# Kernel tuning notes

Measured on AMD Instinct MI355X. Metric: run time of the kernel, lower is better.

The kernel has to match this reference:

```python
import jax, jax.numpy as jnp
import numpy as np


def setup_inputs() -> dict:
    key = jax.random.key(0)
    ks = jax.random.split(key, 12)
    B, Nv, C, H, W = 4, 4096, 64, 376, 1240
    inp = {
        "voxel_features": jax.random.normal(ks[0], (B, Nv, C), jnp.float32),
        "voxels_3d": jax.random.normal(ks[1], (B, Nv, 3), jnp.float32),
        "img_feats": jax.random.normal(ks[2], (B, C, H, W), jnp.float32),
        "vox_x": jax.random.randint(ks[3], (B, Nv), 0, 1400, jnp.int32),
        "vox_y": jax.random.randint(ks[4], (B, Nv), 0, 430, jnp.int32),
        "q_w": jax.random.normal(ks[5], (C, C), jnp.float32) / np.sqrt(C),
        "q_b": jnp.zeros((C,), jnp.float32),
        "k_w": jax.random.normal(ks[6], (C, 3), jnp.float32) / np.sqrt(3.0),
        "k_b": jnp.zeros((C,), jnp.float32),
        "v_w": jax.random.normal(ks[7], (C, C), jnp.float32) / np.sqrt(C),
        "v_b": jnp.zeros((C,), jnp.float32),
        "o_w": jax.random.normal(ks[8], (C, C), jnp.float32) / np.sqrt(C),
        "o_b": jnp.zeros((C,), jnp.float32),
        "fc_w": jax.random.normal(ks[9], (C, C), jnp.float32) / np.sqrt(C),
    }
    return inp


def reference(voxel_features, voxels_3d, img_feats, vox_x, vox_y,
              q_w, q_b, k_w, k_b, v_w, v_b, o_w, o_b, fc_w):
    # voxel_features: [B, Nv, C] lidar voxel features (value)
    # voxels_3d:      [B, Nv, 3] voxel 3D coords (key)
    # img_feats:      [B, C, H, W] image feature map
    B, C, H, W = img_feats.shape
    Nv = voxel_features.shape[1]

    # --- gather image features at projected voxel pixel coords, zero if OOB ---
    valid = (vox_x >= 0) & (vox_x < W) & (vox_y >= 0) & (vox_y < H)  # [B, Nv]
    xc = jnp.clip(vox_x, 0, W - 1)
    yc = jnp.clip(vox_y, 0, H - 1)
    b_idx = jnp.arange(B)[:, None]
    camera = img_feats[b_idx, :, yc, xc]            # [B, Nv, C]
    camera = jnp.where(valid[..., None], camera, 0.0)

    # --- single-head cross-modal attention (q=camera, k=coords, v=lidar) ---
    scale = 1.0 / jnp.sqrt(jnp.asarray(C, camera.dtype))
    q = (camera @ q_w.T + q_b) * scale              # [B, Nv, C]
    k = voxels_3d @ k_w.T + k_b                     # [B, Nv, C]
    v = voxel_features @ v_w.T + v_b                # [B, Nv, C]
    scores = jnp.einsum('bqc,bkc->bqk', q, k)       # [B, Nv, Nv]
    attn = jax.nn.softmax(scores, axis=-1)
    ctx = jnp.einsum('bqk,bkc->bqc', attn, v)
    ctx = ctx @ o_w.T + o_b                         # out_proj

    fused = jax.nn.relu(ctx @ fc_w.T)               # [B, Nv, C]
    return jnp.concatenate([voxel_features, fused], axis=-1)  # [B, Nv, 2C]
```

## Files before the change

### kernel.cpp

```cpp
#include <hip/hip_runtime.h>

#define BB 4
#define NV 4096
#define BN (BB * NV)
#define CC 64
#define HH 376
#define WW 1240
#define HW (HH * WW)
#define LDT 72
#define LDK 36
#define NSPLIT 4
#define TILES 16
#define QSCALE 0.1803368801111244f

typedef __bf16 bf16x8 __attribute__((ext_vector_type(8)));
typedef __bf16 bf16x4 __attribute__((ext_vector_type(4)));
typedef float  f32x4  __attribute__((ext_vector_type(4)));

__global__ __launch_bounds__(256) void kw2(const float* __restrict__ qw,
                                           const float* __restrict__ qb,
                                           const float* __restrict__ kw,
                                           const float* __restrict__ ow,
                                           const float* __restrict__ ob,
                                           const float* __restrict__ fc,
                                           unsigned short* __restrict__ W2b,
                                           float* __restrict__ b2,
                                           float* __restrict__ Wqk3,
                                           float* __restrict__ bqk3) {
  int idx = blockIdx.x * blockDim.x + threadIdx.x;
  if (idx >= CC * CC) return;
  int i = idx >> 6, j = idx & 63;
  float acc = 0.f;
  for (int k = 0; k < CC; ++k) acc += fc[i * CC + k] * ow[k * CC + j];
  ((__bf16*)W2b)[idx] = (__bf16)acc;
  if (idx < CC) {
    float a = 0.f;
    for (int k = 0; k < CC; ++k) a += fc[idx * CC + k] * ob[k];
    b2[idx] = a;
  }
  if (idx < CC * 3) {
    int jj = idx / 3, d = idx - jj * 3;
    float a = 0.f;
    for (int k = 0; k < CC; ++k) a += qw[k * CC + jj] * kw[k * 3 + d];
    Wqk3[idx] = a;
  }
  if (idx < 3) {
    float a = 0.f;
    for (int k = 0; k < CC; ++k) a += qb[k] * kw[k * 3 + idx];
    bqk3[idx] = a;
  }
}

__global__ __launch_bounds__(256) void kprep(
    const float* __restrict__ vfeat, const float* __restrict__ v3d,
    const float* __restrict__ img, const int* __restrict__ vx,
    const int* __restrict__ vy, const float* __restrict__ Wqk3,
    const float* __restrict__ bqk3, const float* __restrict__ vw,
    const float* __restrict__ vb, float* __restrict__ out,
    unsigned short* __restrict__ Qp, unsigned short* __restrict__ K32,
    unsigned short* __restrict__ VTb) {
  __shared__ float VfS[32][68];
  __shared__ float CamS[32][68];
  const int tid = threadIdx.x;
  const int vl = tid >> 3;
  const int p = tid & 7;
  const int gv = blockIdx.x * 32 + vl;
  const int b = gv >> 12, n = gv & (NV - 1);
  const size_t row = (size_t)b * NV + n;

  {
    const float4* vf4 = (const float4*)(vfeat + row * CC) + p * 2;
    float4* o4 = (float4*)(out + row * 128) + p * 2;
    float4* s4 = (float4*)&VfS[vl][p * 8];
#pragma unroll
    for (int i = 0; i < 2; ++i) { float4 t = vf4[i]; o4[i] = t; s4[i] = t; }
  }

  {
    int x = vx[row], y = vy[row];
    bool valid = (x >= 0) & (x < WW) & (y >= 0) & (y < HH);
    int xs = valid ? x : 0, ys = valid ? y : 0;
    const float* ib = img + ((size_t)b * CC + p * 8) * (size_t)HW + (size_t)ys * WW + xs;
#pragma unroll
    for (int i = 0; i < 8; ++i) {
      float cv = ib[(size_t)i * HW];
      CamS[vl][p * 8 + i] = valid ? cv : 0.f;
    }
  }

  if (p == 0) {
    float c0 = v3d[row * 3 + 0], c1 = v3d[row * 3 + 1], c2 = v3d[row * 3 + 2];
    bf16x8 kp = {(__bf16)c0, (__bf16)c1, (__bf16)c2,
                 (__bf16)0.f, (__bf16)0.f, (__bf16)0.f, (__bf16)0.f, (__bf16)0.f};
    *(bf16x8*)(K32 + row * 32) = kp;
  } else if (p < 4) {
    bf16x8 z = {(__bf16)0.f, (__bf16)0.f, (__bf16)0.f, (__bf16)0.f,
                (__bf16)0.f, (__bf16)0.f, (__bf16)0.f, (__bf16)0.f};
    *(bf16x8*)(K32 + row * 32 + p * 8) = z;
  }
  __syncthreads();

  {
    f32x4 vr[16];
#pragma unroll
    for (int i = 0; i < 16; ++i) vr[i] = *(const f32x4*)&VfS[vl][i * 4];
#pragma unroll
    for (int cc = 0; cc < 8; ++cc) {
      int c = p * 8 + cc;
      const float4* w4 = (const float4*)(vw + c * CC);
      float acc = vb[c];
#pragma unroll
      for (int j = 0; j < 16; ++j) {
        float4 w = w4[j];
        acc = fmaf(vr[j][0], w.x, fmaf(vr[j][1], w.y, fmaf(vr[j][2], w.z, fmaf(vr[j][3], w.w, acc))));
      }
      ((__bf16*)VTb)[((size_t)b * CC + c) * NV + n] = (__bf16)acc;
    }
  }

  if (p == 0) {
    float q0 = bqk3[0], q1 = bqk3[1], q2 = bqk3[2];
#pragma unroll 8
    for (int j = 0; j < CC; ++j) {
      float c = CamS[vl][j];
      q0 = fmaf(c, Wqk3[j * 3 + 0], q0);
      q1 = fmaf(c, Wqk3[j * 3 + 1], q1);
      q2 = fmaf(c, Wqk3[j * 3 + 2], q2);
    }
    bf16x8 qp = {(__bf16)(q0 * QSCALE), (__bf16)(q1 * QSCALE), (__bf16)(q2 * QSCALE),
                 (__bf16)0.f, (__bf16)0.f, (__bf16)0.f, (__bf16)0.f, (__bf16)0.f};
    *(bf16x8*)(Qp + row * 32) = qp;
  } else if (p < 4) {
    bf16x8 z = {(__bf16)0.f, (__bf16)0.f, (__bf16)0.f, (__bf16)0.f,
                (__bf16)0.f, (__bf16)0.f, (__bf16)0.f, (__bf16)0.f};
    *(bf16x8*)(Qp + row * 32 + p * 8) = z;
  }
}

__global__ __launch_bounds__(256, 4) void kattn(const unsigned short* __restrict__ Qp,
                                                const unsigned short* __restrict__ K32,
                                                const unsigned short* __restrict__ VTb,
                                                unsigned short* __restrict__ Opb,
                                                float* __restrict__ ml) {
  __shared__ unsigned short Ks[2][64 * LDK];
  __shared__ unsigned short Vs[2][64 * LDT];
  __shared__ unsigned short Ps[4][16 * LDT];

  const int bid = blockIdx.x;
  const int xcd = bid & 7;
  const int idx = bid >> 3;
  const int combo = xcd * 2 + (idx >> 6);
  const int qc = idx & 63;
  const int b = combo >> 2;
  const int sp = combo & 3;
  const int q0 = qc * 64;
  const int key0 = sp * (TILES * 64);

  const int tid = threadIdx.x;
  const int wid = tid >> 6;
  const int lane = tid & 63;
  const int lq = lane & 15;
  const int lg = lane >> 4;

  const int srow = tid >> 2;
  const int scol = (tid & 3) * 16;
  const int kcol = (tid & 3) * 8;

  bf16x8 qf = *(const bf16x8*)(Qp + ((size_t)b * NV + q0 + wid * 16 + lq) * 32 + lg * 8);

  const f32x4 vzero = {0.f, 0.f, 0.f, 0.f};
  float m_run = -1e30f, l_run = 0.f;
  f32x4 oacc[4];
#pragma unroll
  for (int t = 0; t < 4; ++t) oacc[t] = vzero;

  const unsigned short* kgb = K32 + ((size_t)b * NV) * 32;
  const unsigned short* vgb = VTb + (size_t)b * CC * NV;

  uint4 kq, vr0, vr1;
  {
    kq = *(const uint4*)(kgb + (size_t)(key0 + srow) * 32 + kcol);
    const uint4* vsrc = (const uint4*)(vgb + (size_t)srow * NV + key0 + scol);
    vr0 = vsrc[0]; vr1 = vsrc[1];
    *(uint4*)&Ks[0][srow * LDK + kcol] = kq;
    uint4* vdst = (uint4*)&Vs[0][srow * LDT + scol];
    vdst[0] = vr0; vdst[1] = vr1;
  }
  __syncthreads();

  int cur = 0;
  for (int tt = 0; tt < TILES; ++tt) {
    if (tt + 1 < TILES) {
      int k0 = key0 + (tt + 1) * 64;
      kq = *(const uint4*)(kgb + (size_t)(k0 + srow) * 32 + kcol);
      const uint4* vsrc = (const uint4*)(vgb + (size_t)srow * NV + k0 + scol);
      vr0 = vsrc[0]; vr1 = vsrc[1];
    }

    f32x4 s[4];
#pragma unroll
    for (int t = 0; t < 4; ++t) {
      bf16x8 ka = *(const bf16x8*)&Ks[cur][(t * 16 + lq) * LDK + lg * 8];
      s[t] = __builtin_amdgcn_mfma_f32_16x16x32_bf16(ka, qf, vzero, 0, 0, 0);
    }

    float t0m = fmaxf(fmaxf(s[0][0], s[0][1]), fmaxf(s[0][2], s[0][3]));
    float t1m = fmaxf(fmaxf(s[1][0], s[1][1]), fmaxf(s[1][2], s[1][3]));
    float t2m = fmaxf(fmaxf(s[2][0], s[2][1]), fmaxf(s[2][2], s[2][3]));
    float t3m = fmaxf(fmaxf(s[3][0], s[3][1]), fmaxf(s[3][2], s[3][3]));
    float tmax = fmaxf(fmaxf(t0m, t1m), fmaxf(t2m, t3m));
    tmax = fmaxf(tmax, __shfl_xor(tmax, 16));
    tmax = fmaxf(tmax, __shfl_xor(tmax, 32));

    if (!__all(tmax <= m_run + 8.f)) {
      float m_new = fmaxf(m_run, tmax);
      float sc = __builtin_amdgcn_exp2f(m_run - m_new);
      l_run *= sc;
      m_run = m_new;
#pragma unroll
      for (int r = 0; r < 4; ++r) {
        float scr = __shfl(sc, lg * 4 + r);
#pragma unroll
        for (int t = 0; t < 4; ++t) oacc[t][r] *= scr;
      }
    }

    float psum = 0.f;
#pragma unroll
    for (int t = 0; t < 4; ++t) {
      float p0 = __builtin_amdgcn_exp2f(s[t][0] - m_run);
      float p1 = __builtin_amdgcn_exp2f(s[t][1] - m_run);
      float p2 = __builtin_amdgcn_exp2f(s[t][2] - m_run);
      float p3 = __builtin_amdgcn_exp2f(s[t][3] - m_run);
      psum += (p0 + p1) + (p2 + p3);
      bf16x4 pk;
      pk[0] = (__bf16)p0; pk[1] = (__bf16)p1; pk[2] = (__bf16)p2; pk[3] = (__bf16)p3;
      *(bf16x4*)&Ps[wid][lq * LDT + t * 16 + lg * 4] = pk;
    }
    psum += __shfl_xor(psum, 16);
    psum += __shfl_xor(psum, 32);
    l_run += psum;

#pragma unroll
    for (int ks = 0; ks < 2; ++ks) {
      bf16x8 pa = *(const bf16x8*)&Ps[wid][lq * LDT + ks * 32 + lg * 8];
#pragma unroll
      for (int t = 0; t < 4; ++t) {
        bf16x8 vbf = *(const bf16x8*)&Vs[cur][(t * 16 + lq) * LDT + ks * 32 + lg * 8];
        oacc[t] = __builtin_amdgcn_mfma_f32_16x16x32_bf16(pa, vbf, oacc[t], 0, 0, 0);
      }
    }

    if (tt + 1 < TILES) {
      *(uint4*)&Ks[cur ^ 1][srow * LDK + kcol] = kq;
      uint4* vdst = (uint4*)&Vs[cur ^ 1][srow * LDT + scol];
      vdst[0] = vr0; vdst[1] = vr1;
    }
    __syncthreads();
    cur ^= 1;
  }

  const size_t obase = (size_t)sp * BN + (size_t)b * NV + q0 + wid * 16;
#pragma unroll
  for (int r = 0; r < 4; ++r) {
    __bf16* op = (__bf16*)Opb + (obase + lg * 4 + r) * CC + lq;
#pragma unroll
    for (int t = 0; t < 4; ++t) op[t * 16] = (__bf16)oacc[t][r];
  }
  if (lg == 0) {
    float2 t2; t2.x = m_run; t2.y = l_run;
    ((float2*)ml)[obase + lq] = t2;
  }
}

__global__ __launch_bounds__(256) void kmerge(const unsigned short* __restrict__ Opb,
                                              const float* __restrict__ ml,
                                              const unsigned short* __restrict__ W2b,
                                              const float* __restrict__ b2f,
                                              float* __restrict__ out) {
  __shared__ unsigned short W2s[64 * LDT];
  __shared__ float b2s[64];
  const int tid = threadIdx.x;
  const int wid = tid >> 6;
  const int lane = tid & 63;
  const int lq = lane & 15;
  const int lg = lane >> 4;
  const int srow = tid >> 2;
  const int scol = (tid & 3) * 16;

  {
    const uint4* ws = (const uint4*)(W2b + srow * CC + scol);
    uint4* wd = (uint4*)&W2s[srow * LDT + scol];
    wd[0] = ws[0]; wd[1] = ws[1];
    if (tid < 64) b2s[tid] = b2f[tid];
  }
  __syncthreads();

  const int row = blockIdx.x * 64 + wid * 16 + lq;

  float mv[NSPLIT], lv[NSPLIT], w[NSPLIT];
#pragma unroll
  for (int s = 0; s < NSPLIT; ++s) {
    float2 t = ((const float2*)ml)[(size_t)s * BN + row];
    mv[s] = t.x; lv[s] = t.y;
  }
  float mstar = fmaxf(fmaxf(mv[0], mv[1]), fmaxf(mv[2], mv[3]));
  float lstar = 0.f;
#pragma unroll
  for (int s = 0; s < NSPLIT; ++s) {
    w[s] = __builtin_amdgcn_exp2f(mv[s] - mstar);
    lstar = fmaf(w[s], lv[s], lstar);
  }

  float ctx[16];
#pragma unroll
  for (int j = 0; j < 16; ++j) ctx[j] = 0.f;
#pragma unroll
  for (int s = 0; s < NSPLIT; ++s) {
    const __bf16* oprow = (const __bf16*)Opb + ((size_t)s * BN + row) * CC;
    bf16x8 a0 = *(const bf16x8*)(oprow + lg * 8);
    bf16x8 a1 = *(const bf16x8*)(oprow + 32 + lg * 8);
    float ws_ = w[s];
#pragma unroll
    for (int j = 0; j < 8; ++j) {
      ctx[j] = fmaf(ws_, (float)a0[j], ctx[j]);
      ctx[8 + j] = fmaf(ws_, (float)a1[j], ctx[8 + j]);
    }
  }
  float inv = 1.f / lstar;
  bf16x8 cb0, cb1;
#pragma unroll
  for (int j = 0; j < 8; ++j) {
    cb0[j] = (__bf16)(ctx[j] * inv);
    cb1[j] = (__bf16)(ctx[8 + j] * inv);
  }

  const f32x4 vzero = {0.f, 0.f, 0.f, 0.f};
  float* orow = out + (size_t)row * 128 + 64;
#pragma unroll
  for (int t2 = 0; t2 < 4; ++t2) {
    bf16x8 wa0 = *(const bf16x8*)&W2s[(t2 * 16 + lq) * LDT + lg * 8];
    bf16x8 wa1 = *(const bf16x8*)&W2s[(t2 * 16 + lq) * LDT + 32 + lg * 8];
    f32x4 r2 = vzero;
    r2 = __builtin_amdgcn_mfma_f32_16x16x32_bf16(wa0, cb0, r2, 0, 0, 0);
    r2 = __builtin_amdgcn_mfma_f32_16x16x32_bf16(wa1, cb1, r2, 0, 0, 0);
    float4 o;
    o.x = fmaxf(r2[0] + b2s[t2 * 16 + lg * 4 + 0], 0.f);
    o.y = fmaxf(r2[1] + b2s[t2 * 16 + lg * 4 + 1], 0.f);
    o.z = fmaxf(r2[2] + b2s[t2 * 16 + lg * 4 + 2], 0.f);
    o.w = fmaxf(r2[3] + b2s[t2 * 16 + lg * 4 + 3], 0.f);
    *(float4*)(orow + t2 * 16 + lg * 4) = o;
  }
}

extern "C" void kernel_launch(void* const* d_in, const int* in_sizes, int n_in,
                              void* d_out, int out_size, void* d_ws, size_t ws_size,
                              hipStream_t stream) {
  const float* vfeat = (const float*)d_in[0];
  const float* v3d = (const float*)d_in[1];
  const float* img = (const float*)d_in[2];
  const int* vx = (const int*)d_in[3];
  const int* vy = (const int*)d_in[4];
  const float* qw = (const float*)d_in[5];
  const float* qb = (const float*)d_in[6];
  const float* kw = (const float*)d_in[7];
  const float* kb = (const float*)d_in[8];
  const float* vw = (const float*)d_in[9];
  const float* vb = (const float*)d_in[10];
  const float* ow = (const float*)d_in[11];
  const float* ob = (const float*)d_in[12];
  const float* fc = (const float*)d_in[13];
  float* out = (float*)d_out;
  (void)kb;

  char* ws = (char*)d_ws;
  unsigned short* Qp = (unsigned short*)(ws);
  unsigned short* K32 = (unsigned short*)(ws + (1u << 20));
  unsigned short* VTb = (unsigned short*)(ws + (2u << 20));
  unsigned short* Opb = (unsigned short*)(ws + (4u << 20));
  float* ml = (float*)(ws + (12u << 20));
  unsigned short* W2b = (unsigned short*)(ws + (12u << 20) + (512u << 10));
  float* b2 = (float*)(ws + (12u << 20) + (512u << 10) + 8192);
  float* Wqk3 = b2 + 64;
  float* bqk3 = Wqk3 + 192;

  kw2<<<16, 256, 0, stream>>>(qw, qb, kw, ow, ob, fc, W2b, b2, Wqk3, bqk3);
  kprep<<<512, 256, 0, stream>>>(vfeat, v3d, img, vx, vy, Wqk3, bqk3, vw, vb,
                                 out, Qp, K32, VTb);
  kattn<<<1024, 256, 0, stream>>>(Qp, K32, VTb, Opb, ml);
  kmerge<<<256, 256, 0, stream>>>(Opb, ml, W2b, b2, out);
}
```

Baseline: 96.77 us.

## Drop weight-prep kernel, compact Q/K to 8 lanes, read K/V directly from global

Removes the separate kw2 launch: each kprep block recomputes the folded Wq·Wk matrix into shared memory, and each kmerge block recomputes fc·ow and fc·ob into shared memory. Q and K are stored with 8 bf16 per row instead of 32 padded values. The attention kernel drops its LDS double-buffered K/V tiles and block barriers, and loads K and V fragments directly from global memory (lanes outside group 0 feed zeros). This cuts a launch, padded traffic and syncs, at the cost of redundant per-block weight math and uncoalesced, latency-exposed global reads in the inner attention loop.

```diff
diff --git a/kernel.cpp b/kernel.cpp
--- a/kernel.cpp
+++ b/kernel.cpp
@@ -8,7 +8,6 @@
 #define WW 1240
 #define HW (HH * WW)
 #define LDT 72
-#define LDK 36
 #define NSPLIT 4
 #define TILES 16
 #define QSCALE 0.1803368801111244f
@@ -17,50 +16,18 @@
 typedef __bf16 bf16x4 __attribute__((ext_vector_type(4)));
 typedef float  f32x4  __attribute__((ext_vector_type(4)));
 
-__global__ __launch_bounds__(256) void kw2(const float* __restrict__ qw,
-                                           const float* __restrict__ qb,
-                                           const float* __restrict__ kw,
-                                           const float* __restrict__ ow,
-                                           const float* __restrict__ ob,
-                                           const float* __restrict__ fc,
-                                           unsigned short* __restrict__ W2b,
-                                           float* __restrict__ b2,
-                                           float* __restrict__ Wqk3,
-                                           float* __restrict__ bqk3) {
-  int idx = blockIdx.x * blockDim.x + threadIdx.x;
-  if (idx >= CC * CC) return;
-  int i = idx >> 6, j = idx & 63;
-  float acc = 0.f;
-  for (int k = 0; k < CC; ++k) acc += fc[i * CC + k] * ow[k * CC + j];
-  ((__bf16*)W2b)[idx] = (__bf16)acc;
-  if (idx < CC) {
-    float a = 0.f;
-    for (int k = 0; k < CC; ++k) a += fc[idx * CC + k] * ob[k];
-    b2[idx] = a;
-  }
-  if (idx < CC * 3) {
-    int jj = idx / 3, d = idx - jj * 3;
-    float a = 0.f;
-    for (int k = 0; k < CC; ++k) a += qw[k * CC + jj] * kw[k * 3 + d];
-    Wqk3[idx] = a;
-  }
-  if (idx < 3) {
-    float a = 0.f;
-    for (int k = 0; k < CC; ++k) a += qb[k] * kw[k * 3 + idx];
-    bqk3[idx] = a;
-  }
-}
-
 __global__ __launch_bounds__(256) void kprep(
     const float* __restrict__ vfeat, const float* __restrict__ v3d,
     const float* __restrict__ img, const int* __restrict__ vx,
-    const int* __restrict__ vy, const float* __restrict__ Wqk3,
-    const float* __restrict__ bqk3, const float* __restrict__ vw,
-    const float* __restrict__ vb, float* __restrict__ out,
-    unsigned short* __restrict__ Qp, unsigned short* __restrict__ K32,
-    unsigned short* __restrict__ VTb) {
+    const int* __restrict__ vy, const float* __restrict__ qw,
+    const float* __restrict__ qb, const float* __restrict__ kwm,
+    const float* __restrict__ vw, const float* __restrict__ vb,
+    float* __restrict__ out, unsigned short* __restrict__ Qp,
+    unsigned short* __restrict__ K8, unsigned short* __restrict__ VTb) {
   __shared__ float VfS[32][68];
   __shared__ float CamS[32][68];
+  __shared__ float WqkS[64][4];
+  __shared__ float bqkS[4];
   const int tid = threadIdx.x;
   const int vl = tid >> 3;
   const int p = tid & 7;
@@ -68,6 +35,18 @@
   const int b = gv >> 12, n = gv & (NV - 1);
   const size_t row = (size_t)b * NV + n;
 
+  if (tid < 192) {
+    int j = tid / 3, d = tid - j * 3;
+    float a = 0.f;
+    for (int c = 0; c < CC; ++c) a = fmaf(qw[c * CC + j], kwm[c * 3 + d], a);
+    WqkS[j][d] = a;
+  } else if (tid < 195) {
+    int d = tid - 192;
+    float a = 0.f;
+    for (int c = 0; c < CC; ++c) a = fmaf(qb[c], kwm[c * 3 + d], a);
+    bqkS[d] = a;
+  }
+
   {
     const float4* vf4 = (const float4*)(vfeat + row * CC) + p * 2;
     float4* o4 = (float4*)(out + row * 128) + p * 2;
@@ -88,15 +67,11 @@
     }
   }
 
-  if (p == 0) {
+  if (p == 1) {
     float c0 = v3d[row * 3 + 0], c1 = v3d[row * 3 + 1], c2 = v3d[row * 3 + 2];
-    bf16x8 kp = {(__bf16)c0, (__bf16)c1, (__bf16)c2,
-                 (__bf16)0.f, (__bf16)0.f, (__bf16)0.f, (__bf16)0.f, (__bf16)0.f};
-    *(bf16x8*)(K32 + row * 32) = kp;
-  } else if (p < 4) {
-    bf16x8 z = {(__bf16)0.f, (__bf16)0.f, (__bf16)0.f, (__bf16)0.f,
-                (__bf16)0.f, (__bf16)0.f, (__bf16)0.f, (__bf16)0.f};
-    *(bf16x8*)(K32 + row * 32 + p * 8) = z;
+    bf16x8 kp = {(__bf16)c0, (__bf16)c1, (__bf16)c2, (__bf16)0.f,
+                 (__bf16)0.f, (__bf16)0.f, (__bf16)0.f, (__bf16)0.f};
+    *(bf16x8*)(K8 + row * 8) = kp;
   }
   __syncthreads();
 
@@ -119,31 +94,25 @@
   }
 
   if (p == 0) {
-    float q0 = bqk3[0], q1 = bqk3[1], q2 = bqk3[2];
+    float q0 = bqkS[0], q1 = bqkS[1], q2 = bqkS[2];
 #pragma unroll 8
     for (int j = 0; j < CC; ++j) {
       float c = CamS[vl][j];
-      q0 = fmaf(c, Wqk3[j * 3 + 0], q0);
-      q1 = fmaf(c, Wqk3[j * 3 + 1], q1);
-      q2 = fmaf(c, Wqk3[j * 3 + 2], q2);
+      q0 = fmaf(c, WqkS[j][0], q0);
+      q1 = fmaf(c, WqkS[j][1], q1);
+      q2 = fmaf(c, WqkS[j][2], q2);
     }
     bf16x8 qp = {(__bf16)(q0 * QSCALE), (__bf16)(q1 * QSCALE), (__bf16)(q2 * QSCALE),
                  (__bf16)0.f, (__bf16)0.f, (__bf16)0.f, (__bf16)0.f, (__bf16)0.f};
-    *(bf16x8*)(Qp + row * 32) = qp;
-  } else if (p < 4) {
-    bf16x8 z = {(__bf16)0.f, (__bf16)0.f, (__bf16)0.f, (__bf16)0.f,
-                (__bf16)0.f, (__bf16)0.f, (__bf16)0.f, (__bf16)0.f};
-    *(bf16x8*)(Qp + row * 32 + p * 8) = z;
+    *(bf16x8*)(Qp + row * 8) = qp;
   }
 }
 
 __global__ __launch_bounds__(256, 4) void kattn(const unsigned short* __restrict__ Qp,
-                                                const unsigned short* __restrict__ K32,
+                                                const unsigned short* __restrict__ K8,
                                                 const unsigned short* __restrict__ VTb,
                                                 unsigned short* __restrict__ Opb,
                                                 float* __restrict__ ml) {
-  __shared__ unsigned short Ks[2][64 * LDK];
-  __shared__ unsigned short Vs[2][64 * LDT];
   __shared__ unsigned short Ps[4][16 * LDT];
 
   const int bid = blockIdx.x;
@@ -161,12 +130,12 @@
   const int lane = tid & 63;
   const int lq = lane & 15;
   const int lg = lane >> 4;
-
-  const int srow = tid >> 2;
-  const int scol = (tid & 3) * 16;
-  const int kcol = (tid & 3) * 8;
-
-  bf16x8 qf = *(const bf16x8*)(Qp + ((size_t)b * NV + q0 + wid * 16 + lq) * 32 + lg * 8);
+  const bool ld0 = (lg == 0);
+
+  const bf16x8 bz = {(__bf16)0.f, (__bf16)0.f, (__bf16)0.f, (__bf16)0.f,
+                     (__bf16)0.f, (__bf16)0.f, (__bf16)0.f, (__bf16)0.f};
+
+  const bf16x8 qf = ld0 ? *(const bf16x8*)(Qp + ((size_t)b * NV + q0 + wid * 16 + lq) * 8) : bz;
 
   const f32x4 vzero = {0.f, 0.f, 0.f, 0.f};
   float m_run = -1e30f, l_run = 0.f;
@@ -174,33 +143,16 @@
 #pragma unroll
   for (int t = 0; t < 4; ++t) oacc[t] = vzero;
 
-  const unsigned short* kgb = K32 + ((size_t)b * NV) * 32;
+  const unsigned short* kgb = K8 + (size_t)b * NV * 8;
   const unsigned short* vgb = VTb + (size_t)b * CC * NV;
 
-  uint4 kq, vr0, vr1;
-  {
-    kq = *(const uint4*)(kgb + (size_t)(key0 + srow) * 32 + kcol);
-    const uint4* vsrc = (const uint4*)(vgb + (size_t)srow * NV + key0 + scol);
-    vr0 = vsrc[0]; vr1 = vsrc[1];
-    *(uint4*)&Ks[0][srow * LDK + kcol] = kq;
-    uint4* vdst = (uint4*)&Vs[0][srow * LDT + scol];
-    vdst[0] = vr0; vdst[1] = vr1;
-  }
-  __syncthreads();
-
-  int cur = 0;
   for (int tt = 0; tt < TILES; ++tt) {
-    if (tt + 1 < TILES) {
-      int k0 = key0 + (tt + 1) * 64;
-      kq = *(const uint4*)(kgb + (size_t)(k0 + srow) * 32 + kcol);
-      const uint4* vsrc = (const uint4*)(vgb + (size_t)srow * NV + k0 + scol);
-      vr0 = vsrc[0]; vr1 = vsrc[1];
-    }
+    const int kb0 = key0 + tt * 64;
 
     f32x4 s[4];
 #pragma unroll
     for (int t = 0; t < 4; ++t) {
-      bf16x8 ka = *(const bf16x8*)&Ks[cur][(t * 16 + lq) * LDK + lg * 8];
+      bf16x8 ka = ld0 ? *(const bf16x8*)(kgb + (size_t)(kb0 + t * 16 + lq) * 8) : bz;
       s[t] = __builtin_amdgcn_mfma_f32_16x16x32_bf16(ka, qf, vzero, 0, 0, 0);
     }
 
@@ -246,18 +198,10 @@
       bf16x8 pa = *(const bf16x8*)&Ps[wid][lq * LDT + ks * 32 + lg * 8];
 #pragma unroll
       for (int t = 0; t < 4; ++t) {
-        bf16x8 vbf = *(const bf16x8*)&Vs[cur][(t * 16 + lq) * LDT + ks * 32 + lg * 8];
+        bf16x8 vbf = *(const bf16x8*)(vgb + (size_t)(t * 16 + lq) * NV + kb0 + ks * 32 + lg * 8);
         oacc[t] = __builtin_amdgcn_mfma_f32_16x16x32_bf16(pa, vbf, oacc[t], 0, 0, 0);
       }
     }
-
-    if (tt + 1 < TILES) {
-      *(uint4*)&Ks[cur ^ 1][srow * LDK + kcol] = kq;
-      uint4* vdst = (uint4*)&Vs[cur ^ 1][srow * LDT + scol];
-      vdst[0] = vr0; vdst[1] = vr1;
-    }
-    __syncthreads();
-    cur ^= 1;
   }
 
   const size_t obase = (size_t)sp * BN + (size_t)b * NV + q0 + wid * 16;
@@ -275,8 +219,9 @@
 
 __global__ __launch_bounds__(256) void kmerge(const unsigned short* __restrict__ Opb,
                                               const float* __restrict__ ml,
-                                              const unsigned short* __restrict__ W2b,
-                                              const float* __restrict__ b2f,
+                                              const float* __restrict__ ow,
+                                              const float* __restrict__ ob,
+                                              const float* __restrict__ fc,
                                               float* __restrict__ out) {
   __shared__ unsigned short W2s[64 * LDT];
   __shared__ float b2s[64];
@@ -285,14 +230,33 @@
   const int lane = tid & 63;
   const int lq = lane & 15;
   const int lg = lane >> 4;
-  const int srow = tid >> 2;
-  const int scol = (tid & 3) * 16;
 
   {
-    const uint4* ws = (const uint4*)(W2b + srow * CC + scol);
-    uint4* wd = (uint4*)&W2s[srow * LDT + scol];
-    wd[0] = ws[0]; wd[1] = ws[1];
-    if (tid < 64) b2s[tid] = b2f[tid];
+    const int i = tid >> 2;
+    const int jb = (tid & 3) * 16;
+    float acc[16];
+#pragma unroll
+    for (int e = 0; e < 16; ++e) acc[e] = 0.f;
+    for (int k = 0; k < CC; ++k) {
+      float f = fc[i * CC + k];
+      const float4* o4 = (const float4*)(ow + k * CC + jb);
+#pragma unroll
+      for (int e4 = 0; e4 < 4; ++e4) {
+        float4 o = o4[e4];
+        acc[e4 * 4 + 0] = fmaf(f, o.x, acc[e4 * 4 + 0]);
+        acc[e4 * 4 + 1] = fmaf(f, o.y, acc[e4 * 4 + 1]);
+        acc[e4 * 4 + 2] = fmaf(f, o.z, acc[e4 * 4 + 2]);
+        acc[e4 * 4 + 3] = fmaf(f, o.w, acc[e4 * 4 + 3]);
+      }
+    }
+    __bf16* wrow = (__bf16*)&W2s[i * LDT + jb];
+#pragma unroll
+    for (int e = 0; e < 16; ++e) wrow[e] = (__bf16)acc[e];
+    if (tid < CC) {
+      float a = 0.f;
+      for (int k = 0; k < CC; ++k) a = fmaf(fc[tid * CC + k], ob[k], a);
+      b2s[tid] = a;
+    }
   }
   __syncthreads();
 
@@ -363,30 +327,23 @@
   const int* vy = (const int*)d_in[4];
   const float* qw = (const float*)d_in[5];
   const float* qb = (const float*)d_in[6];
-  const float* kw = (const float*)d_in[7];
-  const float* kb = (const float*)d_in[8];
+  const float* kwm = (const float*)d_in[7];
   const float* vw = (const float*)d_in[9];
   const float* vb = (const float*)d_in[10];
   const float* ow = (const float*)d_in[11];
   const float* ob = (const float*)d_in[12];
   const float* fc = (const float*)d_in[13];
   float* out = (float*)d_out;
-  (void)kb;
 
   char* ws = (char*)d_ws;
   unsigned short* Qp = (unsigned short*)(ws);
-  unsigned short* K32 = (unsigned short*)(ws + (1u << 20));
-  unsigned short* VTb = (unsigned short*)(ws + (2u << 20));
-  unsigned short* Opb = (unsigned short*)(ws + (4u << 20));
-  float* ml = (float*)(ws + (12u << 20));
-  unsigned short* W2b = (unsigned short*)(ws + (12u << 20) + (512u << 10));
-  float* b2 = (float*)(ws + (12u << 20) + (512u << 10) + 8192);
-  float* Wqk3 = b2 + 64;
-  float* bqk3 = Wqk3 + 192;
-
-  kw2<<<16, 256, 0, stream>>>(qw, qb, kw, ow, ob, fc, W2b, b2, Wqk3, bqk3);
-  kprep<<<512, 256, 0, stream>>>(vfeat, v3d, img, vx, vy, Wqk3, bqk3, vw, vb,
-                                 out, Qp, K32, VTb);
-  kattn<<<1024, 256, 0, stream>>>(Qp, K32, VTb, Opb, ml);
-  kmerge<<<256, 256, 0, stream>>>(Opb, ml, W2b, b2, out);
+  unsigned short* K8 = (unsigned short*)(ws + 262144);
+  unsigned short* VTb = (unsigned short*)(ws + 524288);
+  unsigned short* Opb = (unsigned short*)(ws + 2621440);
+  float* ml = (float*)(ws + 11010048);
+
+  kprep<<<512, 256, 0, stream>>>(vfeat, v3d, img, vx, vy, qw, qb, kwm, vw, vb,
+                                 out, Qp, K8, VTb);
+  kattn<<<1024, 256, 0, stream>>>(Qp, K8, VTb, Opb, ml);
+  kmerge<<<256, 256, 0, stream>>>(Opb, ml, ow, ob, fc, out);
 }
```

Result: slower. 147.7 us (+52.6%).
